# Kernel tuning notes

Hardware: AMD Instinct MI355X
Metric: run time of the kernel (lower is better)

The kernel has to match this reference:

```python
import jax, jax.numpy as jnp
import numpy as np

V, E, D, T, B = 32000, 512, 512, 512, 32
PAD = 3

def layer_norm(x, g, b, eps=1e-5):
    m = jnp.mean(x, axis=-1, keepdims=True)
    v = jnp.mean((x - m) ** 2, axis=-1, keepdims=True)
    return (x - m) * jax.lax.rsqrt(v + eps) * g + b

def sru_direction(U, v, b, reverse):
    # U: (T, B, 4D) -> splits: x_tilde, f-gate pre-act, r-gate pre-act, highway input
    x_t, uf, ur, xp = jnp.split(U, 4, axis=-1)
    def step(c, inp):
        xt, uft, urt, xpt = inp
        f = jax.nn.sigmoid(uft + v[0] * c + b[0])
        r = jax.nn.sigmoid(urt + v[1] * c + b[1])
        c_new = f * c + (1.0 - f) * xt
        h = r * c_new + (1.0 - r) * xpt
        return c_new, h
    c0 = jnp.zeros((U.shape[1], v.shape[1]), U.dtype)  # (B, D)
    c_last, hs = jax.lax.scan(step, c0, (x_t, uf, ur, xp), reverse=reverse)
    return hs, c_last

def setup_inputs() -> dict:
    key = jax.random.key(0)
    ks = jax.random.split(key, 8)
    def rn(k, shp, sc=0.05):
        return jax.random.normal(k, shp, jnp.float32) * sc
    return {
        "src": jax.random.randint(ks[0], (T, B), 0, V),
        "emb": rn(ks[1], (V, E), 0.1),
        "ln_g": jnp.ones((E,), jnp.float32),
        "ln_b": jnp.zeros((E,), jnp.float32),
        "W0": rn(ks[2], (E, 4 * D)),
        "W1": rn(ks[3], (E, 4 * D)),
        "v0": rn(ks[4], (2, D), 0.5),
        "v1": rn(ks[5], (2, D), 0.5),
        "b0": jnp.zeros((2, D), jnp.float32),
        "b1": jnp.zeros((2, D), jnp.float32),
        "W_out": rn(ks[6], (D, 2 * D)),
        "b_out": jnp.zeros((D,), jnp.float32),
    }

def reference(src, emb, ln_g, ln_b, W0, W1, v0, v1, b0, b1, W_out, b_out):
    table = emb.at[PAD].set(0.0)          # padding_idx row is zero
    x = table[src]                         # (T, B, E); dropout p=0 -> identity
    xn = layer_norm(x, ln_g, ln_b)         # SRU layer_norm=True: LN on cell input
    h0, c0 = sru_direction(jnp.einsum('tbe,ef->tbf', xn, W0), v0, b0, False)
    h1, c1 = sru_direction(jnp.einsum('tbe,ef->tbf', xn, W1), v1, b1, True)
    outputs = jnp.concatenate([h0, h1], axis=-1)        # (T, B, 2D)
    hidden = jnp.concatenate([c0, c1], axis=-1)[None]   # (1, B, 2D)
    out = jnp.tanh(jnp.einsum('tbh,dh->tbd', outputs, W_out) + b_out)
    return out, hidden
```

## Files before the change

kernel.cpp:

```cpp
#include <hip/hip_runtime.h>
#include <cstdint>
#include <cstddef>

#define T_DIM 512
#define B_DIM 32
#define E_DIM 512
#define D_DIM 512
#define PAD_IDX 3
#define M_ROWS (T_DIM * B_DIM)
#define PF 32

typedef __attribute__((ext_vector_type(8))) __bf16 bf16x8;
typedef __attribute__((ext_vector_type(4))) float  f32x4;

__device__ __forceinline__ unsigned short f2bf(float x) {
    union { float f; uint32_t u; } v; v.f = x;
    uint32_t u = v.u;
    uint32_t r = (u + 0x7FFFu + ((u >> 16) & 1u)) >> 16;
    return (unsigned short)r;
}
__device__ __forceinline__ float bf2f(unsigned short h) {
    union { float f; uint32_t u; } v; v.u = ((uint32_t)h) << 16;
    return v.f;
}
__device__ __forceinline__ float fast_sigmoid(float z) {
    return __builtin_amdgcn_rcpf(1.f + __expf(-z));
}
__device__ __forceinline__ float fast_tanh(float x) {
    return 1.f - 2.f * __builtin_amdgcn_rcpf(__expf(2.f * x) + 1.f);
}

__global__ __launch_bounds__(256) void wconv_kernel(
    const float* __restrict__ W0, const float* __restrict__ W1,
    unsigned short* __restrict__ Wt)
{
    __shared__ float tile[64][65];
    int k0  = blockIdx.x * 64;
    int n0g = blockIdx.y * 64;
    int dir = n0g >> 11;
    const float* W = dir ? W1 : W0;
    int d0 = (n0g & 2047) >> 2;
    int tx = threadIdx.x & 63;
    int ty = threadIdx.x >> 6;
    int scol = ((tx >> 4) << 9) + d0 + (tx & 15);
    for (int r = ty; r < 64; r += 4)
        tile[r][tx] = W[(size_t)(k0 + r) * 2048 + scol];
    __syncthreads();
    for (int r2 = ty; r2 < 64; r2 += 4) {
        int j = ((r2 & 3) << 4) | (r2 >> 2);
        Wt[(size_t)(n0g + r2) * 512 + k0 + tx] = f2bf(tile[tx][j]);
    }
}

__global__ __launch_bounds__(256) void bias_build_kernel(
    const float* __restrict__ b0, const float* __restrict__ b1,
    float* __restrict__ bias)
{
    int n = blockIdx.x * 256 + threadIdx.x;
    int dir = n >> 11, g = n & 3, d = (n & 2047) >> 2;
    const float* bp = dir ? b1 : b0;
    float v = (g == 1) ? bp[d] : ((g == 2) ? bp[512 + d] : 0.f);
    bias[n] = v;
}

__global__ __launch_bounds__(256) void woutconv_kernel(
    const float* __restrict__ W, unsigned short* __restrict__ O)
{
    int i = (blockIdx.x * 256 + threadIdx.x) * 4;
    f32x4 v = *(const f32x4*)(W + i);
    uint2 pk;
    pk.x = (uint32_t)f2bf(v[0]) | ((uint32_t)f2bf(v[1]) << 16);
    pk.y = (uint32_t)f2bf(v[2]) | ((uint32_t)f2bf(v[3]) << 16);
    *(uint2*)(O + i) = pk;
}

__global__ __launch_bounds__(256) void embed_ln_kernel(
    const int* __restrict__ src, const float* __restrict__ emb,
    const float* __restrict__ g, const float* __restrict__ bb,
    unsigned short* __restrict__ xn)
{
    int wave = threadIdx.x >> 6;
    int lane = threadIdx.x & 63;
    int row  = blockIdx.x * 4 + wave;
    int tok  = src[row];
    float x[8];
    if (tok == PAD_IDX) {
        #pragma unroll
        for (int j = 0; j < 8; j++) x[j] = 0.f;
    } else {
        const float* er = emb + (size_t)tok * E_DIM + lane * 8;
        f32x4 a0 = *(const f32x4*)(er);
        f32x4 a1 = *(const f32x4*)(er + 4);
        #pragma unroll
        for (int j = 0; j < 4; j++) { x[j] = a0[j]; x[4 + j] = a1[j]; }
    }
    float s = 0.f, sq = 0.f;
    #pragma unroll
    for (int j = 0; j < 8; j++) { s += x[j]; sq += x[j] * x[j]; }
    #pragma unroll
    for (int off = 32; off >= 1; off >>= 1) {
        s  += __shfl_xor(s,  off, 64);
        sq += __shfl_xor(sq, off, 64);
    }
    float mean = s * (1.f / 512.f);
    float var  = sq * (1.f / 512.f) - mean * mean;
    float rs   = rsqrtf(var + 1e-5f);
    f32x4 g0 = *(const f32x4*)(g + lane * 8);
    f32x4 g1 = *(const f32x4*)(g + lane * 8 + 4);
    f32x4 b0 = *(const f32x4*)(bb + lane * 8);
    f32x4 b1 = *(const f32x4*)(bb + lane * 8 + 4);
    unsigned short o[8];
    #pragma unroll
    for (int j = 0; j < 4; j++) {
        o[j]     = f2bf((x[j]     - mean) * rs * g0[j] + b0[j]);
        o[4 + j] = f2bf((x[4 + j] - mean) * rs * g1[j] + b1[j]);
    }
    uint4 pk;
    pk.x = (uint32_t)o[0] | ((uint32_t)o[1] << 16);
    pk.y = (uint32_t)o[2] | ((uint32_t)o[3] << 16);
    pk.z = (uint32_t)o[4] | ((uint32_t)o[5] << 16);
    pk.w = (uint32_t)o[6] | ((uint32_t)o[7] << 16);
    *(uint4*)(xn + (size_t)row * E_DIM + lane * 8) = pk;
}

template <int KD, int EPI>
__global__ __launch_bounds__(256) void gemm_kernel(
    const unsigned short* __restrict__ A,
    const unsigned short* __restrict__ Bt,
    void* __restrict__ Cout,
    const float* __restrict__ bias,
    int ldc)
{
    __shared__ unsigned short Al[128 * 64];
    __shared__ unsigned short Bl[128 * 64];
    const int tid  = threadIdx.x;
    const int wave = tid >> 6;
    const int lane = tid & 63;
    const int mt = blockIdx.y, nt = blockIdx.x;
    const int wm = wave >> 1, wn = wave & 1;

    f32x4 acc[4][4];
    #pragma unroll
    for (int m = 0; m < 4; m++)
        #pragma unroll
        for (int n = 0; n < 4; n++)
            acc[m][n] = (f32x4){0.f, 0.f, 0.f, 0.f};

    const unsigned short* Abase = A  + (size_t)(mt * 128) * KD;
    const unsigned short* Bbase = Bt + (size_t)(nt * 128) * KD;
    const int lrow = lane >> 3;
    const int lcol = (lane & 7) ^ lrow;

    for (int kt = 0; kt < KD; kt += 64) {
        const unsigned short* Ag = Abase + kt;
        const unsigned short* Bg = Bbase + kt;
        #pragma unroll
        for (int i = 0; i < 4; i++) {
            int c   = wave * 4 + i;
            int row = c * 8 + lrow;
            __builtin_amdgcn_global_load_lds(
                (const __attribute__((address_space(1))) void*)(Ag + (size_t)row * KD + lcol * 8),
                (__attribute__((address_space(3))) void*)(Al + c * 512),
                16, 0, 0);
        }
        #pragma unroll
        for (int i = 0; i < 4; i++) {
            int c   = wave * 4 + i;
            int row = c * 8 + lrow;
            __builtin_amdgcn_global_load_lds(
                (const __attribute__((address_space(1))) void*)(Bg + (size_t)row * KD + lcol * 8),
                (__attribute__((address_space(3))) void*)(Bl + c * 512),
                16, 0, 0);
        }
        __syncthreads();

        #pragma unroll
        for (int kk = 0; kk < 2; kk++) {
            const int cg = kk * 4 + (lane >> 4);
            bf16x8 af[4], bfv[4];
            #pragma unroll
            for (int m = 0; m < 4; m++) {
                int row = wm * 64 + m * 16 + (lane & 15);
                af[m] = *(const bf16x8*)(Al + row * 64 + ((cg ^ (row & 7)) * 8));
            }
            #pragma unroll
            for (int n = 0; n < 4; n++) {
                int row = wn * 64 + n * 16 + (lane & 15);
                bfv[n] = *(const bf16x8*)(Bl + row * 64 + ((cg ^ (row & 7)) * 8));
            }
            #pragma unroll
            for (int m = 0; m < 4; m++)
                #pragma unroll
                for (int n = 0; n < 4; n++)
                    acc[m][n] = __builtin_amdgcn_mfma_f32_16x16x32_bf16(
                        af[m], bfv[n], acc[m][n], 0, 0, 0);
        }
        __syncthreads();
    }

    const int colb = nt * 128 + wn * 64;
    const int rowb = mt * 128 + wm * 64;
    #pragma unroll
    for (int m = 0; m < 4; m++) {
        #pragma unroll
        for (int n = 0; n < 4; n++) {
            int col  = colb + n * 16 + (lane & 15);
            int row0 = rowb + m * 16 + (lane >> 4) * 4;
            float bi = bias[col];
            if (EPI == 0) {
                unsigned short* C = (unsigned short*)Cout;
                #pragma unroll
                for (int j = 0; j < 4; j++)
                    C[(size_t)(row0 + j) * ldc + col] = f2bf(acc[m][n][j] + bi);
            } else {
                float* C = (float*)Cout;
                #pragma unroll
                for (int j = 0; j < 4; j++)
                    C[(size_t)(row0 + j) * ldc + col] = fast_tanh(acc[m][n][j] + bi);
            }
        }
    }
}

__global__ __launch_bounds__(64) void sru_scan_kernel(
    const unsigned short* __restrict__ U,
    const float* __restrict__ v0, const float* __restrict__ v1,
    unsigned short* __restrict__ h,
    float* __restrict__ hidden)
{
    int id  = blockIdx.x * 64 + threadIdx.x;
    int dir = id >> 14;
    int rem = id & 16383;
    int b   = rem >> 9;
    int d   = rem & 511;
    const float* v = dir ? v1 : v0;
    float vf = v[d], vr = v[D_DIM + d];

    int row0  = (dir ? (T_DIM - 1) * B_DIM : 0) + b;
    long step = (long)(dir ? -B_DIM : B_DIM) * 1024;

    const ushort4* lp = (const ushort4*)U + (size_t)row0 * 1024 + dir * 512 + d;
    unsigned short* hp = h + (size_t)row0 * 1024 + dir * 512 + d;

    ushort4 buf[PF];
    #pragma unroll
    for (int p = 0; p < PF; p++) { buf[p] = *lp; lp += step; }

    float c = 0.f;
    for (int tb = 0; tb < T_DIM - PF; tb += PF) {
        #pragma unroll
        for (int p = 0; p < PF; p++) {
            ushort4 q = buf[p];
            buf[p] = *lp; lp += step;
            float x  = bf2f(q.x);
            float uf = bf2f(q.y);
            float ur = bf2f(q.z);
            float xp = bf2f(q.w);
            float f = fast_sigmoid(__fmaf_rn(vf, c, uf));
            float r = fast_sigmoid(__fmaf_rn(vr, c, ur));
            c = __fmaf_rn(f, c - x, x);
            float hv = __fmaf_rn(r, c - xp, xp);
            *hp = f2bf(hv); hp += step;
        }
    }
    #pragma unroll
    for (int p = 0; p < PF; p++) {
        ushort4 q = buf[p];
        float x  = bf2f(q.x);
        float uf = bf2f(q.y);
        float ur = bf2f(q.z);
        float xp = bf2f(q.w);
        float f = fast_sigmoid(__fmaf_rn(vf, c, uf));
        float r = fast_sigmoid(__fmaf_rn(vr, c, ur));
        c = __fmaf_rn(f, c - x, x);
        float hv = __fmaf_rn(r, c - xp, xp);
        *hp = f2bf(hv); hp += step;
    }
    hidden[b * 1024 + dir * 512 + d] = c;
}

extern "C" void kernel_launch(void* const* d_in, const int* in_sizes, int n_in,
                              void* d_out, int out_size, void* d_ws, size_t ws_size,
                              hipStream_t stream)
{
    const int*   src   = (const int*)  d_in[0];
    const float* emb   = (const float*)d_in[1];
    const float* ln_g  = (const float*)d_in[2];
    const float* ln_b  = (const float*)d_in[3];
    const float* W0    = (const float*)d_in[4];
    const float* W1    = (const float*)d_in[5];
    const float* v0    = (const float*)d_in[6];
    const float* v1    = (const float*)d_in[7];
    const float* b0    = (const float*)d_in[8];
    const float* b1    = (const float*)d_in[9];
    const float* W_out = (const float*)d_in[10];
    const float* b_out = (const float*)d_in[11];

    unsigned short* Wt  = (unsigned short*)d_ws;
    unsigned short* Wob = Wt  + (size_t)4096 * 512;
    unsigned short* xn  = Wob + (size_t)512 * 1024;
    unsigned short* U   = xn  + (size_t)M_ROWS * 512;
    unsigned short* h   = U   + (size_t)M_ROWS * 4096;
    float*          bias4096 = (float*)(h + (size_t)M_ROWS * 1024);

    float* out    = (float*)d_out;
    float* hidden = out + (size_t)M_ROWS * D_DIM;

    wconv_kernel<<<dim3(8, 64), 256, 0, stream>>>(W0, W1, Wt);
    bias_build_kernel<<<16, 256, 0, stream>>>(b0, b1, bias4096);
    woutconv_kernel<<<512, 256, 0, stream>>>(W_out, Wob);
    embed_ln_kernel<<<M_ROWS / 4, 256, 0, stream>>>(src, emb, ln_g, ln_b, xn);

    gemm_kernel<512, 0><<<dim3(32, 128), 256, 0, stream>>>(xn, Wt, (void*)U, bias4096, 4096);

    sru_scan_kernel<<<512, 64, 0, stream>>>(U, v0, v1, h, hidden);

    gemm_kernel<1024, 1><<<dim3(4, 128), 256, 0, stream>>>(h, Wob, (void*)d_out, b_out, 512);
}
```

Measured before the change: 185.5 us.

## Replace GEMM with multi-stage pipelined LDS kernel using larger tiles and swizzled grid

Rewrites the bf16 MFMA GEMM to use a 4-deep ring of LDS buffers with K-step 32. Three stages are prefetched, and explicit vmcnt waits and barriers overlap global-to-LDS loads with MFMA compute. Tiles grow to 256x256 (input projection) and 256x128 (output projection) with 512-thread blocks. A block-index swizzle improves L2 locality, and setprio raises MFMA priority. The large LDS footprint limits occupancy, and hand-written waitcnt logic adds correctness risk.

New measurement: 174.2 us. 1.06x faster.

```diff
diff --git a/kernel.cpp b/kernel.cpp
--- a/kernel.cpp
+++ b/kernel.cpp
@@ -123,89 +123,114 @@
     *(uint4*)(xn + (size_t)row * E_DIM + lane * 8) = pk;
 }
 
-template <int KD, int EPI>
-__global__ __launch_bounds__(256) void gemm_kernel(
+template<int BM, int BN, int WM, int WN, int KD, int LOGNT, int EPI>
+__global__ __launch_bounds__(512, 2) void gemm_pipe_kernel(
     const unsigned short* __restrict__ A,
     const unsigned short* __restrict__ Bt,
     void* __restrict__ Cout,
     const float* __restrict__ bias,
     int ldc)
 {
-    __shared__ unsigned short Al[128 * 64];
-    __shared__ unsigned short Bl[128 * 64];
-    const int tid  = threadIdx.x;
-    const int wave = tid >> 6;
-    const int lane = tid & 63;
-    const int mt = blockIdx.y, nt = blockIdx.x;
-    const int wm = wave >> 1, wn = wave & 1;
-
-    f32x4 acc[4][4];
-    #pragma unroll
-    for (int m = 0; m < 4; m++)
-        #pragma unroll
-        for (int n = 0; n < 4; n++)
+    constexpr int NKT = KD / 32;
+    constexpr int MR  = BM / WM / 16;
+    constexpr int NR  = BN / WN / 16;
+    constexpr int RA  = BM / 128;
+    constexpr int RB  = BN / 128;
+    constexpr int LPT = RA + RB;
+    constexpr int ASZ = BM * 32;
+    constexpr int BSZ = BN * 32;
+    __shared__ unsigned short smem[4 * (ASZ + BSZ)];
+
+    const int tid = threadIdx.x;
+    const int w   = tid >> 6;
+    const int l   = tid & 63;
+
+    const int bid = blockIdx.x;
+    const int cpx = gridDim.x >> 3;
+    const int swz = (bid & 7) * cpx + (bid >> 3);
+    const int mt  = swz >> LOGNT;
+    const int nt  = swz & ((1 << LOGNT) - 1);
+
+    const int wm = w / WN, wn = w % WN;
+
+    const unsigned short* Ab = A  + (size_t)mt * BM * KD;
+    const unsigned short* Bb = Bt + (size_t)nt * BN * KD;
+
+    const int srow = w * 16 + (l >> 2);
+    const int scol = ((l & 3) ^ ((l >> 3) & 3)) * 8;
+
+    auto stage = [&](int t) {
+        const unsigned short* Ag = Ab + t * 32;
+        const unsigned short* Bg = Bb + t * 32;
+        unsigned short* As = smem + (t & 3) * (ASZ + BSZ);
+        unsigned short* Bs = As + ASZ;
+        #pragma unroll
+        for (int r = 0; r < RA; r++)
+            __builtin_amdgcn_global_load_lds(
+                (const __attribute__((address_space(1))) void*)(Ag + (size_t)(r * 128 + srow) * KD + scol),
+                (__attribute__((address_space(3))) void*)(As + (r * 128 + w * 16) * 32),
+                16, 0, 0);
+        #pragma unroll
+        for (int r = 0; r < RB; r++)
+            __builtin_amdgcn_global_load_lds(
+                (const __attribute__((address_space(1))) void*)(Bg + (size_t)(r * 128 + srow) * KD + scol),
+                (__attribute__((address_space(3))) void*)(Bs + (r * 128 + w * 16) * 32),
+                16, 0, 0);
+    };
+
+    f32x4 acc[MR][NR];
+    #pragma unroll
+    for (int m = 0; m < MR; m++)
+        #pragma unroll
+        for (int n = 0; n < NR; n++)
             acc[m][n] = (f32x4){0.f, 0.f, 0.f, 0.f};
 
-    const unsigned short* Abase = A  + (size_t)(mt * 128) * KD;
-    const unsigned short* Bbase = Bt + (size_t)(nt * 128) * KD;
-    const int lrow = lane >> 3;
-    const int lcol = (lane & 7) ^ lrow;
-
-    for (int kt = 0; kt < KD; kt += 64) {
-        const unsigned short* Ag = Abase + kt;
-        const unsigned short* Bg = Bbase + kt;
-        #pragma unroll
-        for (int i = 0; i < 4; i++) {
-            int c   = wave * 4 + i;
-            int row = c * 8 + lrow;
-            __builtin_amdgcn_global_load_lds(
-                (const __attribute__((address_space(1))) void*)(Ag + (size_t)row * KD + lcol * 8),
-                (__attribute__((address_space(3))) void*)(Al + c * 512),
-                16, 0, 0);
+    stage(0); stage(1); stage(2);
+
+    const int li   = l & 15;
+    const int cg   = l >> 4;
+    const int rswz = (cg ^ ((li >> 1) & 3)) * 8;
+
+    for (int t = 0; t < NKT; t++) {
+        __builtin_amdgcn_sched_barrier(0);
+        if (t + 2 < NKT)      asm volatile("s_waitcnt vmcnt(%0)" :: "n"(2 * LPT) : "memory");
+        else if (t + 1 < NKT) asm volatile("s_waitcnt vmcnt(%0)" :: "n"(LPT) : "memory");
+        else                  asm volatile("s_waitcnt vmcnt(0)" ::: "memory");
+        __builtin_amdgcn_s_barrier();
+        __builtin_amdgcn_sched_barrier(0);
+        if (t + 3 < NKT) stage(t + 3);
+
+        const unsigned short* As = smem + (t & 3) * (ASZ + BSZ);
+        const unsigned short* Bs = As + ASZ;
+        bf16x8 af[MR], bfv[NR];
+        #pragma unroll
+        for (int m = 0; m < MR; m++) {
+            int row = wm * (BM / WM) + m * 16 + li;
+            af[m] = *(const bf16x8*)(As + row * 32 + rswz);
         }
         #pragma unroll
-        for (int i = 0; i < 4; i++) {
-            int c   = wave * 4 + i;
-            int row = c * 8 + lrow;
-            __builtin_amdgcn_global_load_lds(
-                (const __attribute__((address_space(1))) void*)(Bg + (size_t)row * KD + lcol * 8),
-                (__attribute__((address_space(3))) void*)(Bl + c * 512),
-                16, 0, 0);
+        for (int n = 0; n < NR; n++) {
+            int row = wn * (BN / WN) + n * 16 + li;
+            bfv[n] = *(const bf16x8*)(Bs + row * 32 + rswz);
         }
-        __syncthreads();
-
-        #pragma unroll
-        for (int kk = 0; kk < 2; kk++) {
-            const int cg = kk * 4 + (lane >> 4);
-            bf16x8 af[4], bfv[4];
+        __builtin_amdgcn_s_setprio(1);
+        #pragma unroll
+        for (int m = 0; m < MR; m++)
             #pragma unroll
-            for (int m = 0; m < 4; m++) {
-                int row = wm * 64 + m * 16 + (lane & 15);
-                af[m] = *(const bf16x8*)(Al + row * 64 + ((cg ^ (row & 7)) * 8));
-            }
-            #pragma unroll
-            for (int n = 0; n < 4; n++) {
-                int row = wn * 64 + n * 16 + (lane & 15);
-                bfv[n] = *(const bf16x8*)(Bl + row * 64 + ((cg ^ (row & 7)) * 8));
-            }
-            #pragma unroll
-            for (int m = 0; m < 4; m++)
-                #pragma unroll
-                for (int n = 0; n < 4; n++)
-                    acc[m][n] = __builtin_amdgcn_mfma_f32_16x16x32_bf16(
-                        af[m], bfv[n], acc[m][n], 0, 0, 0);
-        }
-        __syncthreads();
-    }
-
-    const int colb = nt * 128 + wn * 64;
-    const int rowb = mt * 128 + wm * 64;
-    #pragma unroll
-    for (int m = 0; m < 4; m++) {
-        #pragma unroll
-        for (int n = 0; n < 4; n++) {
-            int col  = colb + n * 16 + (lane & 15);
-            int row0 = rowb + m * 16 + (lane >> 4) * 4;
+            for (int n = 0; n < NR; n++)
+                acc[m][n] = __builtin_amdgcn_mfma_f32_16x16x32_bf16(
+                    af[m], bfv[n], acc[m][n], 0, 0, 0);
+        __builtin_amdgcn_s_setprio(0);
+    }
+
+    const int colb = nt * BN + wn * (BN / WN);
+    const int rowb = mt * BM + wm * (BM / WM);
+    #pragma unroll
+    for (int m = 0; m < MR; m++) {
+        #pragma unroll
+        for (int n = 0; n < NR; n++) {
+            int col  = colb + n * 16 + li;
+            int row0 = rowb + m * 16 + cg * 4;
             float bi = bias[col];
             if (EPI == 0) {
                 unsigned short* C = (unsigned short*)Cout;
@@ -305,15 +330,18 @@
 
     float* out    = (float*)d_out;
     float* hidden = out + (size_t)M_ROWS * D_DIM;
+    (void)out;
 
     wconv_kernel<<<dim3(8, 64), 256, 0, stream>>>(W0, W1, Wt);
     bias_build_kernel<<<16, 256, 0, stream>>>(b0, b1, bias4096);
     woutconv_kernel<<<512, 256, 0, stream>>>(W_out, Wob);
     embed_ln_kernel<<<M_ROWS / 4, 256, 0, stream>>>(src, emb, ln_g, ln_b, xn);
 
-    gemm_kernel<512, 0><<<dim3(32, 128), 256, 0, stream>>>(xn, Wt, (void*)U, bias4096, 4096);
+    gemm_pipe_kernel<256, 256, 2, 4, 512, 4, 0>
+        <<<1024, 512, 0, stream>>>(xn, Wt, (void*)U, bias4096, 4096);
 
     sru_scan_kernel<<<512, 64, 0, stream>>>(U, v0, v1, h, hidden);
 
-    gemm_kernel<1024, 1><<<dim3(4, 128), 256, 0, stream>>>(h, Wob, (void*)d_out, b_out, 512);
-}
+    gemm_pipe_kernel<256, 128, 4, 2, 1024, 2, 1>
+        <<<256, 512, 0, stream>>>(h, Wob, (void*)d_out, b_out, 512);
+}
```
